# Kernel optimization log

Measured on AMD Instinct MI355X. Metric: run time of the kernel, lower is better.

## Reference

```python
import jax, jax.numpy as jnp
import numpy as np

B, S, HIDDEN = 1, 2048, 3584
NH, NKV, HD = 16, 8, 256
N_REP = NH // NKV
EPS = 1e-6
SCALING = 256.0 ** -0.5  # query_pre_attn_scalar=256
SOFTCAP = 50.0
NEG = -1e9


def rmsnorm(x, w):
    # Gemma RMSNorm with unit offset, computed in fp32
    xf = x.astype(jnp.float32)
    n = xf * jax.lax.rsqrt(jnp.mean(xf * xf, axis=-1, keepdims=True) + EPS)
    return (n * (1.0 + w.astype(jnp.float32))).astype(x.dtype)


def rope(x, cos, sin):
    # x: [B,S,H,D]; gemma pairs (x[:D/2], x[D/2:]) as complex (rotate-half)
    x1, x2 = jnp.split(x, 2, axis=-1)
    c = cos[None, :, None, :]
    s = sin[None, :, None, :]
    return jnp.concatenate([x1 * c - x2 * s, x1 * s + x2 * c], axis=-1).astype(x.dtype)


def setup_inputs() -> dict:
    key = jax.random.key(0)
    ks = jax.random.split(key, 6)
    hidden_states = jax.random.normal(ks[0], (B, S, HIDDEN), jnp.float32)
    w_qkv = jax.random.normal(ks[1], ((NH + 2 * NKV) * HD, HIDDEN), jnp.float32) * 0.02
    w_o = jax.random.normal(ks[2], (HIDDEN, NH * HD), jnp.float32) * 0.02
    q_norm_w = jax.random.normal(ks[3], (HD,), jnp.float32) * 0.1
    k_norm_w = jax.random.normal(ks[4], (HD,), jnp.float32) * 0.1
    k_cache = jnp.zeros((B, S, NKV, HD), jnp.float32)
    v_cache = jnp.zeros((B, S, NKV, HD), jnp.float32)
    kv_write_indices = jnp.arange(S, dtype=jnp.int32)
    # rotary tables, theta=10000
    inv_freq = 1.0 / (10000.0 ** (np.arange(0, HD, 2, dtype=np.float32) / HD))
    t = np.arange(S, dtype=np.float32)
    freqs = np.outer(t, inv_freq)  # [S, HD/2]
    cos = jnp.asarray(np.cos(freqs), jnp.float32)
    sin = jnp.asarray(np.sin(freqs), jnp.float32)
    # causal additive mask [1,1,S,S]
    causal = np.tril(np.ones((S, S), dtype=bool))
    mask = jnp.asarray(np.where(causal, 0.0, NEG).astype(np.float32))[None, None]
    return {"hidden_states": hidden_states, "cos": cos, "sin": sin,
            "kv_write_indices": kv_write_indices, "k_cache": k_cache,
            "v_cache": v_cache, "mask": mask, "w_qkv": w_qkv, "w_o": w_o,
            "q_norm_w": q_norm_w, "k_norm_w": k_norm_w}


def reference(hidden_states, cos, sin, kv_write_indices, k_cache, v_cache,
              mask, w_qkv, w_o, q_norm_w, k_norm_w):
    qkv = jnp.einsum('bsh,oh->bso', hidden_states, w_qkv)
    q_size, kv_size = NH * HD, NKV * HD
    xq = qkv[..., :q_size].reshape(B, S, NH, HD)
    xk = qkv[..., q_size:q_size + kv_size].reshape(B, S, NKV, HD)
    xv = qkv[..., q_size + kv_size:].reshape(B, S, NKV, HD)
    xq = rmsnorm(xq, q_norm_w)
    xk = rmsnorm(xk, k_norm_w)
    xq = rope(xq, cos, sin)
    xk = rope(xk, cos, sin)
    # KV cache write (index_copy_ along dim 1)
    kc = k_cache.at[:, kv_write_indices].set(xk)
    vc = v_cache.at[:, kv_write_indices].set(xv)
    # GQA expand
    key = jnp.repeat(kc, N_REP, axis=2)   # [B,S,NH,HD]
    val = jnp.repeat(vc, N_REP, axis=2)
    q = xq.transpose(0, 2, 1, 3) * SCALING  # [B,NH,S,HD]
    k = key.transpose(0, 2, 1, 3)
    v = val.transpose(0, 2, 1, 3)
    scores = jnp.einsum('bhqd,bhkd->bhqk', q, k)
    scores = jnp.tanh(scores / SOFTCAP) * SOFTCAP  # logit softcapping
    scores = scores + mask
    p = jax.nn.softmax(scores, axis=-1)
    out = jnp.einsum('bhqk,bhkd->bhqd', p, v)
    out = out.transpose(0, 2, 1, 3).reshape(B, S, NH * HD)
    return jnp.einsum('bsd,hd->bsh', out, w_o)
```

## Files before the change

kernel.cpp:

```cpp
#include <hip/hip_runtime.h>

typedef __bf16 bf16;
typedef __bf16 bf16x4 __attribute__((ext_vector_type(4)));
typedef __bf16 bf16x8 __attribute__((ext_vector_type(8)));
typedef float f32x4 __attribute__((ext_vector_type(4)));

#define S_LEN 2048
#define HID   3584
#define NHEADS 16
#define NKVH   8
#define HDIM   256
#define QKV_O  8192
#define O_IN   4096

typedef const __attribute__((address_space(1))) void* gp_t;
typedef __attribute__((address_space(3))) void* sp_t;

__device__ __forceinline__ void async16(const void* g, void* s) {
  __builtin_amdgcn_global_load_lds((gp_t)g, (sp_t)s, 16, 0, 0);
}

__device__ __forceinline__ f32x4 mfma16(bf16x8 a, bf16x8 b, f32x4 c) {
  return __builtin_amdgcn_mfma_f32_16x16x32_bf16(a, b, c, 0, 0, 0);
}

__global__ __launch_bounds__(256) void cast_kernel(const float* __restrict__ in,
                                                   bf16* __restrict__ out, int n4) {
  int i = blockIdx.x * 256 + threadIdx.x;
  if (i >= n4) return;
  f32x4 v = ((const f32x4*)in)[i];
  bf16x4 o = { (bf16)v[0], (bf16)v[1], (bf16)v[2], (bf16)v[3] };
  ((bf16x4*)out)[i] = o;
}

__global__ __launch_bounds__(256) void gemm_nt(const bf16* __restrict__ A, const bf16* __restrict__ B,
                                               float* __restrict__ C, int M, int N, int K) {
  __shared__ bf16 As[128 * 64];
  __shared__ bf16 Bs[128 * 64];
  int tid = threadIdx.x;
  int lane = tid & 63;
  int bm = blockIdx.y, bn = blockIdx.x;
  int w = tid >> 6, wm = w >> 1, wn = w & 1;
  int fr = lane & 15, fq = lane >> 4;
  int sr = tid >> 3;
  int sc = tid & 7;
  int cg = sc ^ (sr & 7);
  const bf16* Ag = A + (size_t)(bm * 128 + sr) * K + cg * 8;
  const bf16* Bg = B + (size_t)(bn * 128 + sr) * K + cg * 8;
  bf16* Asl = &As[sr * 64 + sc * 8];
  bf16* Bsl = &Bs[sr * 64 + sc * 8];
  const bf16* Af = &As[(wm * 64 + fr) * 64];
  const bf16* Bf = &Bs[(wn * 64 + fr) * 64];
  int fsw = fr & 7;
  int fo0 = ((fq ^ fsw) * 8);
  int fo1 = (((4 + fq) ^ fsw) * 8);
  f32x4 acc[4][4];
#pragma unroll
  for (int i = 0; i < 4; i++)
#pragma unroll
    for (int j = 0; j < 4; j++) { f32x4 z = {0.f, 0.f, 0.f, 0.f}; acc[i][j] = z; }
  for (int k0 = 0; k0 < K; k0 += 64) {
    __syncthreads();
#pragma unroll
    for (int p = 0; p < 4; p++) {
      async16(Ag + k0 + (size_t)(p * 32) * K, Asl + p * 32 * 64);
      async16(Bg + k0 + (size_t)(p * 32) * K, Bsl + p * 32 * 64);
    }
    __syncthreads();
#pragma unroll
    for (int ks = 0; ks < 2; ks++) {
      int fo = ks ? fo1 : fo0;
      bf16x8 a[4], b[4];
#pragma unroll
      for (int t = 0; t < 4; t++) a[t] = *(const bf16x8*)(Af + t * 16 * 64 + fo);
#pragma unroll
      for (int t = 0; t < 4; t++) b[t] = *(const bf16x8*)(Bf + t * 16 * 64 + fo);
#pragma unroll
      for (int i = 0; i < 4; i++)
#pragma unroll
        for (int j = 0; j < 4; j++) acc[i][j] = mfma16(a[i], b[j], acc[i][j]);
    }
  }
  int row0 = bm * 128 + wm * 64 + fq * 4;
  int col0 = bn * 128 + wn * 64 + fr;
#pragma unroll
  for (int i = 0; i < 4; i++)
#pragma unroll
    for (int j = 0; j < 4; j++)
#pragma unroll
      for (int r = 0; r < 4; r++)
        C[(size_t)(row0 + i * 16 + r) * N + col0 + j * 16] = acc[i][j][r];
}

__global__ __launch_bounds__(256) void qk_norm_rope(const float* __restrict__ qkv,
                                                    const float* __restrict__ cosb,
                                                    const float* __restrict__ sinb,
                                                    const float* __restrict__ qw,
                                                    const float* __restrict__ kw,
                                                    bf16* __restrict__ qout,
                                                    bf16* __restrict__ kout) {
  int s = blockIdx.x;
  int lane = threadIdx.x & 63;
  int w = threadIdx.x >> 6;
  int d0 = lane * 4;
  int dr = d0 & 127;
  f32x4 cv = *(const f32x4*)(cosb + s * 128 + dr);
  f32x4 sv = *(const f32x4*)(sinb + s * 128 + dr);
  bool hi = lane >= 32;
#pragma unroll
  for (int r = 0; r < 6; r++) {
    int head = r * 4 + w;
    const float* x = qkv + (size_t)s * QKV_O + head * HDIM + d0;
    f32x4 v = *(const f32x4*)x;
    float ss = v[0] * v[0] + v[1] * v[1] + v[2] * v[2] + v[3] * v[3];
#pragma unroll
    for (int off = 32; off > 0; off >>= 1) ss += __shfl_xor(ss, off);
    float scale = rsqrtf(ss * (1.0f / HDIM) + 1e-6f);
    bool isq = head < NHEADS;
    const float* wn = isq ? qw : kw;
    f32x4 wv = *(const f32x4*)(wn + d0);
    float y[4], o[4];
#pragma unroll
    for (int i = 0; i < 4; i++) y[i] = v[i] * scale * (1.0f + wv[i]);
#pragma unroll
    for (int i = 0; i < 4; i++) {
      float py = __shfl_xor(y[i], 32);
      o[i] = hi ? (py * sv[i] + y[i] * cv[i]) : (y[i] * cv[i] - py * sv[i]);
    }
    float mult = isq ? 0.0625f : 1.0f;
    bf16x4 ov = { (bf16)(o[0] * mult), (bf16)(o[1] * mult), (bf16)(o[2] * mult), (bf16)(o[3] * mult) };
    if (isq) *(bf16x4*)(qout + ((size_t)head * S_LEN + s) * HDIM + d0) = ov;
    else     *(bf16x4*)(kout + ((size_t)(head - NHEADS) * S_LEN + s) * HDIM + d0) = ov;
  }
}

__global__ __launch_bounds__(256) void v_transpose(const float* __restrict__ qkv, bf16* __restrict__ vt) {
  __shared__ float tile[64][65];
  int dt = blockIdx.x, st = blockIdx.y, h = blockIdx.z;
  int t = threadIdx.x;
  int d0 = dt * 64, s0 = st * 64;
#pragma unroll
  for (int i = 0; i < 16; i++) {
    int idx = i * 256 + t;
    int r = idx >> 6, c = idx & 63;
    tile[r][c] = qkv[(size_t)(s0 + r) * QKV_O + 6144 + h * HDIM + d0 + c];
  }
  __syncthreads();
#pragma unroll
  for (int i = 0; i < 16; i++) {
    int idx = i * 256 + t;
    int dr = idx >> 6, sc = idx & 63;
    vt[((size_t)h * HDIM + d0 + dr) * S_LEN + s0 + sc] = (bf16)tile[sc][dr];
  }
}

#define PSTRIDE 40
__global__ __launch_bounds__(256) void attn_kernel(const bf16* __restrict__ q,
                                                   const bf16* __restrict__ kx,
                                                   const bf16* __restrict__ vt,
                                                   bf16* __restrict__ aout) {
  __shared__ bf16 kt[32 * 256];
  __shared__ bf16 vtile[256 * 32];
  __shared__ bf16 pbuf[4][16 * PSTRIDE];
  int h = blockIdx.x;
  int y = blockIdx.y;
  int qt = (y < 16) ? y : 47 - y;
  int kvh = h >> 1;
  int tid = threadIdx.x;
  int lane = tid & 63, w = tid >> 6;
  int fr = lane & 15, fq = lane >> 4;
  int qs = qt * 64;
  bf16x8 qf[8];
  const bf16* qb = q + ((size_t)h * S_LEN + qs + w * 16 + fr) * HDIM + fq * 8;
#pragma unroll
  for (int i = 0; i < 8; i++) qf[i] = *(const bf16x8*)(qb + i * 32);
  f32x4 acc[16];
#pragma unroll
  for (int i = 0; i < 16; i++) { f32x4 z = {0.f, 0.f, 0.f, 0.f}; acc[i] = z; }
  float lsum[4] = {0.f, 0.f, 0.f, 0.f};
  int krow = w * 2 + (lane >> 5);
  int kcolr = (lane & 31) * 8;
  const bf16* kg = kx + (size_t)kvh * S_LEN * HDIM;
  int vd = w * 16 + (lane >> 2);
  int vsw = (vd >> 1) & 3;
  int vcl = (lane & 3) * 8;
  int vcg = (((lane & 3) ^ vsw) * 8);
  const bf16* vg = vt + (size_t)kvh * HDIM * S_LEN;
  int rot0 = (fq * 8 - fr * 8) & 255;
  int rot1 = (fq * 8 - fr * 8 - 128) & 255;
  const bf16* kt0 = &kt[fr * 256];
  const bf16* kt1 = &kt[(16 + fr) * 256];
  int fsw = (fr >> 1) & 3;
  int kmax = qs + 64;
  for (int k0 = 0; k0 < kmax; k0 += 32) {
    __syncthreads();
#pragma unroll
    for (int p = 0; p < 4; p++) {
      int r = p * 8 + krow;
      int gc = (kcolr + r * 8) & 255;
      async16(kg + (size_t)(k0 + r) * HDIM + gc, &kt[r * 256 + kcolr]);
      int d = p * 64 + vd;
      async16(vg + (size_t)d * S_LEN + k0 + vcg, &vtile[d * 32 + vcl]);
    }
    __syncthreads();
    f32x4 s0 = {0.f, 0.f, 0.f, 0.f}, s1 = {0.f, 0.f, 0.f, 0.f};
#pragma unroll
    for (int kk = 0; kk < 8; kk++) {
      bf16x8 b0 = *(const bf16x8*)(kt0 + ((kk * 32 + rot0) & 255));
      bf16x8 b1 = *(const bf16x8*)(kt1 + ((kk * 32 + rot1) & 255));
      s0 = mfma16(qf[kk], b0, s0);
      s1 = mfma16(qf[kk], b1, s1);
    }
#pragma unroll
    for (int reg = 0; reg < 4; reg++) {
      int rowg = qs + w * 16 + fq * 4 + reg;
      float u0 = __builtin_amdgcn_exp2f(0.057707802f * s0[reg]);
      float u1 = __builtin_amdgcn_exp2f(0.057707802f * s1[reg]);
      float p0 = __builtin_amdgcn_exp2f(28.853901f - 144.26950f * __builtin_amdgcn_rcpf(u0 + 1.0f));
      float p1 = __builtin_amdgcn_exp2f(28.853901f - 144.26950f * __builtin_amdgcn_rcpf(u1 + 1.0f));
      p0 = (k0 + fr <= rowg) ? p0 : 0.0f;
      p1 = (k0 + 16 + fr <= rowg) ? p1 : 0.0f;
      lsum[reg] += p0 + p1;
      pbuf[w][(fq * 4 + reg) * PSTRIDE + fr] = (bf16)p0;
      pbuf[w][(fq * 4 + reg) * PSTRIDE + 16 + fr] = (bf16)p1;
    }
    bf16x8 pf = *(const bf16x8*)&pbuf[w][fr * PSTRIDE + fq * 8];
#pragma unroll
    for (int ct = 0; ct < 16; ct++) {
      bf16x8 vf = *(const bf16x8*)&vtile[(ct * 16 + fr) * 32 + (fq ^ fsw) * 8];
      acc[ct] = mfma16(pf, vf, acc[ct]);
    }
  }
  float rl[4];
#pragma unroll
  for (int reg = 0; reg < 4; reg++) {
    float l = lsum[reg];
    l += __shfl_xor(l, 1);
    l += __shfl_xor(l, 2);
    l += __shfl_xor(l, 4);
    l += __shfl_xor(l, 8);
    rl[reg] = 1.0f / l;
  }
#pragma unroll
  for (int ct = 0; ct < 16; ct++)
#pragma unroll
    for (int reg = 0; reg < 4; reg++)
      aout[(size_t)(qs + w * 16 + fq * 4 + reg) * O_IN + h * HDIM + ct * 16 + fr] =
          (bf16)(acc[ct][reg] * rl[reg]);
}

extern "C" void kernel_launch(void* const* d_in, const int* in_sizes, int n_in,
                              void* d_out, int out_size, void* d_ws, size_t ws_size,
                              hipStream_t stream) {
  const float* hidden = (const float*)d_in[0];
  const float* cosb   = (const float*)d_in[1];
  const float* sinb   = (const float*)d_in[2];
  const float* wqkv   = (const float*)d_in[7];
  const float* wo     = (const float*)d_in[8];
  const float* qnw    = (const float*)d_in[9];
  const float* knw    = (const float*)d_in[10];
  float* out = (float*)d_out;
  char* ws = (char*)d_ws;
  bf16*  h_bf    = (bf16*)(ws + 0);
  bf16*  wqkv_bf = (bf16*)(ws + 14680064);
  bf16*  wo_bf   = (bf16*)(ws + 73400320);
  float* qkv     = (float*)(ws + 102760448);
  bf16*  qb      = (bf16*)(ws + 169869312);
  bf16*  kb      = (bf16*)(ws + 186646528);
  bf16*  vtb     = (bf16*)(ws + 195035136);
  bf16*  attnb   = (bf16*)(ws + 203423744);

  cast_kernel<<<7168, 256, 0, stream>>>(hidden, h_bf, 1835008);
  cast_kernel<<<28672, 256, 0, stream>>>(wqkv, wqkv_bf, 7340032);
  cast_kernel<<<14336, 256, 0, stream>>>(wo, wo_bf, 3670016);
  gemm_nt<<<dim3(64, 16), 256, 0, stream>>>(h_bf, wqkv_bf, qkv, 2048, 8192, 3584);
  qk_norm_rope<<<2048, 256, 0, stream>>>(qkv, cosb, sinb, qnw, knw, qb, kb);
  v_transpose<<<dim3(4, 32, 8), 256, 0, stream>>>(qkv, vtb);
  attn_kernel<<<dim3(16, 32), 256, 0, stream>>>(qb, kb, vtb, attnb);
  gemm_nt<<<dim3(28, 16), 256, 0, stream>>>(attnb, wo_bf, out, 2048, 3584, 4096);
}
```

Measured before the change: 652.7 us.

## Add 256x256-tile 8-wave pipelined GEMM for the QKV projection

Adds a new NT GEMM kernel with 256x256 output tiles, 512 threads and double-buffered LDS filled by async global-to-LDS loads, interleaving staging with MFMA phases and raising MFMA wave priority. It also remaps block IDs so neighbouring blocks spread across XCD groups. The QKV projection now uses this kernel in place of the 128x128 one, aiming for higher arithmetic intensity and better overlap of loads with compute. The grid shrinks to 256 blocks, so there is less latency hiding between blocks, the tiles use a lot of LDS and registers, and the fixed barrier schedule is fragile.

New measurement: 614.2 us. 5.9% less time.

```diff
diff --git a/kernel.cpp b/kernel.cpp
--- a/kernel.cpp
+++ b/kernel.cpp
@@ -31,6 +31,135 @@
   f32x4 v = ((const f32x4*)in)[i];
   bf16x4 o = { (bf16)v[0], (bf16)v[1], (bf16)v[2], (bf16)v[3] };
   ((bf16x4*)out)[i] = o;
+}
+
+__global__ __launch_bounds__(512, 2) void gemm_nt_8p(const bf16* __restrict__ A,
+                                                     const bf16* __restrict__ B,
+                                                     float* __restrict__ C,
+                                                     int M, int N, int K) {
+  __shared__ bf16 As0[256 * 64];
+  __shared__ bf16 Bs0[256 * 64];
+  __shared__ bf16 As1[256 * 64];
+  __shared__ bf16 Bs1[256 * 64];
+  int tid = threadIdx.x;
+  int lane = tid & 63;
+  int w = tid >> 6;
+  int wm = w >> 2, wn = w & 3;
+  int nbn = N >> 8;
+  int lid = blockIdx.x;
+  int oid = (lid & 7) * ((int)gridDim.x >> 3) + (lid >> 3);
+  int bm = oid / nbn;
+  int bn = oid - bm * nbn;
+  int srow = tid >> 3, schunk = tid & 7;
+  int gcol = (schunk ^ (srow & 7)) * 8;
+  const bf16* Ag = A + (size_t)(bm * 256 + srow) * K + gcol;
+  const bf16* Bg = B + (size_t)(bn * 256 + srow) * K + gcol;
+  int soff = srow * 64 + schunk * 8;
+  int fr = lane & 15, fq = lane >> 4;
+  int c0 = ((fq) ^ (fr & 7)) * 8;
+  int c1 = ((4 + fq) ^ (fr & 7)) * 8;
+  const int arow = (wm * 128 + fr) * 64;
+  const int brow = (wn * 64 + fr) * 64;
+
+  f32x4 acc[8][4];
+#pragma unroll
+  for (int i = 0; i < 8; i++)
+#pragma unroll
+    for (int j = 0; j < 4; j++) { f32x4 z = {0.f, 0.f, 0.f, 0.f}; acc[i][j] = z; }
+  bf16x8 a[8], b[8];
+
+#define STG(gb, lb, kk, half) do {                                    \
+    const bf16* _g = (gb) + (size_t)((half) * 128) * K + (kk);        \
+    bf16* _l = (lb) + (half) * 128 * 64 + soff;                       \
+    async16(_g, _l);                                                  \
+    async16(_g + (size_t)64 * K, _l + 64 * 64);                       \
+  } while (0)
+#define LDA8(base, mg) do {                                           \
+    const bf16* _p = (base) + arow + (mg) * 64 * 64;                  \
+    _Pragma("unroll")                                                 \
+    for (int i = 0; i < 4; i++) {                                     \
+      a[i * 2 + 0] = *(const bf16x8*)(_p + i * 16 * 64 + c0);         \
+      a[i * 2 + 1] = *(const bf16x8*)(_p + i * 16 * 64 + c1);         \
+    }                                                                 \
+  } while (0)
+#define LDB4(base, jh) do {                                           \
+    const bf16* _p = (base) + brow + (jh) * 32 * 64;                  \
+    _Pragma("unroll")                                                 \
+    for (int j = 0; j < 2; j++) {                                     \
+      b[(jh) * 4 + j * 2 + 0] = *(const bf16x8*)(_p + j * 16 * 64 + c0); \
+      b[(jh) * 4 + j * 2 + 1] = *(const bf16x8*)(_p + j * 16 * 64 + c1); \
+    }                                                                 \
+  } while (0)
+#define MM16(mg, jh) do {                                             \
+    __builtin_amdgcn_s_setprio(1);                                    \
+    _Pragma("unroll")                                                 \
+    for (int i = 0; i < 4; i++) {                                     \
+      acc[(mg) * 4 + i][(jh) * 2 + 0] = mfma16(a[i * 2 + 0], b[(jh) * 4 + 0], acc[(mg) * 4 + i][(jh) * 2 + 0]); \
+      acc[(mg) * 4 + i][(jh) * 2 + 0] = mfma16(a[i * 2 + 1], b[(jh) * 4 + 1], acc[(mg) * 4 + i][(jh) * 2 + 0]); \
+      acc[(mg) * 4 + i][(jh) * 2 + 1] = mfma16(a[i * 2 + 0], b[(jh) * 4 + 2], acc[(mg) * 4 + i][(jh) * 2 + 1]); \
+      acc[(mg) * 4 + i][(jh) * 2 + 1] = mfma16(a[i * 2 + 1], b[(jh) * 4 + 3], acc[(mg) * 4 + i][(jh) * 2 + 1]); \
+    }                                                                 \
+    __builtin_amdgcn_s_setprio(0);                                    \
+  } while (0)
+#define BAR() __builtin_amdgcn_s_barrier()
+#define WAITL() do { asm volatile("s_waitcnt lgkmcnt(0)" ::: "memory"); \
+                     __builtin_amdgcn_sched_barrier(0); } while (0)
+#define WAITV4() asm volatile("s_waitcnt vmcnt(4)" ::: "memory")
+
+  const int nT = K >> 6;
+  const int nIter = K >> 7;
+  STG(Ag, As0, 0, 0); STG(Ag, As0, 0, 1);
+  STG(Bg, Bs0, 0, 0); STG(Bg, Bs0, 0, 1);
+  STG(Bg, Bs1, 64, 0); STG(Bg, Bs1, 64, 1);
+  WAITV4();
+  BAR();
+
+  for (int t = 0; t < nIter; t++) {
+    int T = 2 * t;
+    int kA1 = (T + 1) * 64;
+    int t2 = T + 2; if (t2 > nT - 1) t2 = nT - 1;
+    int t3 = T + 3; if (t3 > nT - 1) t3 = nT - 1;
+    int k2 = t2 * 64, k3 = t3 * 64;
+    LDA8(As0, 0); LDB4(Bs0, 0);
+    STG(Ag, As1, kA1, 0);
+    BAR(); WAITL(); MM16(0, 0); BAR();
+    LDB4(Bs0, 1);
+    STG(Ag, As1, kA1, 1);
+    BAR(); WAITL(); MM16(0, 1); BAR();
+    LDA8(As0, 1);
+    STG(Bg, Bs0, k2, 0);
+    BAR(); WAITL(); MM16(1, 0); BAR();
+    STG(Bg, Bs0, k2, 1);
+    BAR(); MM16(1, 1); WAITV4(); BAR();
+    LDA8(As1, 0); LDB4(Bs1, 0);
+    STG(Ag, As0, k2, 0);
+    BAR(); WAITL(); MM16(0, 0); BAR();
+    LDB4(Bs1, 1);
+    STG(Ag, As0, k2, 1);
+    BAR(); WAITL(); MM16(0, 1); BAR();
+    LDA8(As1, 1);
+    STG(Bg, Bs1, k3, 0);
+    BAR(); WAITL(); MM16(1, 0); BAR();
+    STG(Bg, Bs1, k3, 1);
+    BAR(); MM16(1, 1); WAITV4(); BAR();
+  }
+#undef STG
+#undef LDA8
+#undef LDB4
+#undef MM16
+#undef BAR
+#undef WAITL
+#undef WAITV4
+
+  int row0 = bm * 256 + wm * 128 + fq * 4;
+  int col0 = bn * 256 + wn * 64 + fr;
+#pragma unroll
+  for (int i = 0; i < 8; i++)
+#pragma unroll
+    for (int j = 0; j < 4; j++)
+#pragma unroll
+      for (int r = 0; r < 4; r++)
+        C[(size_t)(row0 + i * 16 + r) * N + col0 + j * 16] = acc[i][j][r];
 }
 
 __global__ __launch_bounds__(256) void gemm_nt(const bf16* __restrict__ A, const bf16* __restrict__ B,
@@ -273,7 +402,7 @@
   cast_kernel<<<7168, 256, 0, stream>>>(hidden, h_bf, 1835008);
   cast_kernel<<<28672, 256, 0, stream>>>(wqkv, wqkv_bf, 7340032);
   cast_kernel<<<14336, 256, 0, stream>>>(wo, wo_bf, 3670016);
-  gemm_nt<<<dim3(64, 16), 256, 0, stream>>>(h_bf, wqkv_bf, qkv, 2048, 8192, 3584);
+  gemm_nt_8p<<<256, 512, 0, stream>>>(h_bf, wqkv_bf, qkv, 2048, 8192, 3584);
   qk_norm_rope<<<2048, 256, 0, stream>>>(qkv, cosb, sinb, qnw, knw, qb, kb);
   v_transpose<<<dim3(4, 32, 8), 256, 0, stream>>>(qkv, vtb);
   attn_kernel<<<dim3(16, 32), 256, 0, stream>>>(qb, kb, vtb, attnb);
```

## Replace GEMMs with 256x256 double-buffered 8-wave pipeline and split-K output projection

Applied to the files above, without the earlier changes.

Replaces the simple 128x128 GEMM with a 512-thread kernel that computes 256x256 tiles. It double-buffers LDS, overlaps async global-to-LDS loads with MFMA work using explicit waitcnt, barriers and setprio, and remaps block IDs so nearby blocks share tiles in cache. The output projection is split into two K halves to fill more CUs, with partial results written to workspace and summed by an extra add kernel. This trades extra fp32 partial-buffer traffic and one more launch for higher MFMA utilisation and better occupancy.

New measurement: 580.0 us. 11.1% less time.

```diff
diff --git a/kernel.cpp b/kernel.cpp
--- a/kernel.cpp
+++ b/kernel.cpp
@@ -33,63 +33,172 @@
   ((bf16x4*)out)[i] = o;
 }
 
-__global__ __launch_bounds__(256) void gemm_nt(const bf16* __restrict__ A, const bf16* __restrict__ B,
-                                               float* __restrict__ C, int M, int N, int K) {
-  __shared__ bf16 As[128 * 64];
-  __shared__ bf16 Bs[128 * 64];
+__global__ __launch_bounds__(256) void add2_kernel(const float* __restrict__ a,
+                                                   const float* __restrict__ b,
+                                                   float* __restrict__ o, int n4) {
+  int i = blockIdx.x * 256 + threadIdx.x;
+  if (i >= n4) return;
+  f32x4 x = ((const f32x4*)a)[i];
+  f32x4 y = ((const f32x4*)b)[i];
+  ((f32x4*)o)[i] = x + y;
+}
+
+#define GSTG(gb, lb, kk, half, LDAB) do {                              \
+    const bf16* _g = (gb) + (size_t)((half) * 128) * (LDAB) + (kk);    \
+    bf16* _l = (lb) + (half) * 128 * 64 + soff;                        \
+    async16(_g, _l);                                                   \
+    async16(_g + (size_t)64 * (LDAB), _l + 64 * 64);                   \
+  } while (0)
+#define LD12(ab, bb, cx, ar, br) do {                                  \
+    const bf16* _pa = (ab) + arow;                                     \
+    const bf16* _pb = (bb) + brow;                                     \
+    _Pragma("unroll")                                                  \
+    for (int _i = 0; _i < 8; _i++) ar[_i] = *(const bf16x8*)(_pa + _i * 16 * 64 + (cx)); \
+    _Pragma("unroll")                                                  \
+    for (int _j = 0; _j < 4; _j++) br[_j] = *(const bf16x8*)(_pb + _j * 16 * 64 + (cx)); \
+  } while (0)
+#define MM32(ar, br) do {                                              \
+    __builtin_amdgcn_s_setprio(1);                                     \
+    _Pragma("unroll")                                                  \
+    for (int _i = 0; _i < 8; _i++)                                     \
+      _Pragma("unroll")                                                \
+      for (int _j = 0; _j < 4; _j++)                                   \
+        acc[_i][_j] = mfma16(ar[_i], br[_j], acc[_i][_j]);             \
+    __builtin_amdgcn_s_setprio(0);                                     \
+  } while (0)
+#define BARS() do { __builtin_amdgcn_s_barrier(); __builtin_amdgcn_sched_barrier(0); } while (0)
+#define LGKM0() asm volatile("s_waitcnt lgkmcnt(0)" ::: "memory")
+#define WAITV8() asm volatile("s_waitcnt vmcnt(8)" ::: "memory")
+
+#define GEMM_PIPE_BODY(LDAB)                                           \
+  f32x4 acc[8][4];                                                     \
+  _Pragma("unroll")                                                    \
+  for (int i = 0; i < 8; i++)                                          \
+    _Pragma("unroll")                                                  \
+    for (int j = 0; j < 4; j++) { f32x4 z = {0.f, 0.f, 0.f, 0.f}; acc[i][j] = z; } \
+  bf16x8 a0[8], b0[4], a1[8], b1[4];                                   \
+  const int nT = K >> 6;                                               \
+  const int nIter = K >> 7;                                            \
+  GSTG(Ag, As0, 0, 0, LDAB); GSTG(Ag, As0, 0, 1, LDAB);                \
+  GSTG(Bg, Bs0, 0, 0, LDAB); GSTG(Bg, Bs0, 0, 1, LDAB);                \
+  GSTG(Ag, As1, 64, 0, LDAB); GSTG(Ag, As1, 64, 1, LDAB);              \
+  GSTG(Bg, Bs1, 64, 0, LDAB); GSTG(Bg, Bs1, 64, 1, LDAB);              \
+  WAITV8();                                                            \
+  BARS();                                                              \
+  LD12(As0, Bs0, c0, a0, b0);                                          \
+  for (int t = 0; t < nIter; t++) {                                    \
+    int t2 = 2 * t + 2; if (t2 > nT - 1) t2 = nT - 1;                  \
+    int t3 = 2 * t + 3; if (t3 > nT - 1) t3 = nT - 1;                  \
+    int k2 = t2 * 64, k3 = t3 * 64;                                    \
+              \
+    LD12(As0, Bs0, c1, a1, b1);                                        \
+    MM32(a0, b0);                                                      \
+    LGKM0();                                                           \
+    BARS();                                                            \
+    \
+    GSTG(Ag, As0, k2, 0, LDAB); GSTG(Ag, As0, k2, 1, LDAB);            \
+    GSTG(Bg, Bs0, k2, 0, LDAB); GSTG(Bg, Bs0, k2, 1, LDAB);            \
+    MM32(a1, b1);                                                      \
+    WAITV8();                                                          \
+    BARS();                                                            \
+    LD12(As1, Bs1, c0, a0, b0);                                        \
+                                             \
+    LD12(As1, Bs1, c1, a1, b1);                                        \
+    MM32(a0, b0);                                                      \
+    LGKM0();                                                           \
+    BARS();                                                            \
+                                                              \
+    GSTG(Ag, As1, k3, 0, LDAB); GSTG(Ag, As1, k3, 1, LDAB);            \
+    GSTG(Bg, Bs1, k3, 0, LDAB); GSTG(Bg, Bs1, k3, 1, LDAB);            \
+    MM32(a1, b1);                                                      \
+    WAITV8();                                                          \
+    BARS();                                                            \
+    LD12(As0, Bs0, c0, a0, b0);                                        \
+  }
+
+__global__ __launch_bounds__(512, 2) void gemm_nt_8p(const bf16* __restrict__ A,
+                                                     const bf16* __restrict__ B,
+                                                     float* __restrict__ C,
+                                                     int M, int N, int K) {
+  __shared__ bf16 As0[256 * 64];
+  __shared__ bf16 Bs0[256 * 64];
+  __shared__ bf16 As1[256 * 64];
+  __shared__ bf16 Bs1[256 * 64];
   int tid = threadIdx.x;
   int lane = tid & 63;
-  int bm = blockIdx.y, bn = blockIdx.x;
-  int w = tid >> 6, wm = w >> 1, wn = w & 1;
+  int w = tid >> 6;
+  int wm = w >> 2, wn = w & 3;
+  int lid = blockIdx.x;
+  int oid = (lid & 7) * 32 + (lid >> 3);
+  int rect = oid >> 5, ri = oid & 31;
+  int bm = (rect & 3) * 2 + (ri >> 4);
+  int bn = (rect >> 2) * 16 + (ri & 15);
+  int srow = tid >> 3, schunk = tid & 7;
+  int gcol = (schunk ^ (srow & 7)) * 8;
+  const bf16* Ag = A + (size_t)(bm * 256 + srow) * K + gcol;
+  const bf16* Bg = B + (size_t)(bn * 256 + srow) * K + gcol;
+  int soff = srow * 64 + schunk * 8;
   int fr = lane & 15, fq = lane >> 4;
-  int sr = tid >> 3;
-  int sc = tid & 7;
-  int cg = sc ^ (sr & 7);
-  const bf16* Ag = A + (size_t)(bm * 128 + sr) * K + cg * 8;
-  const bf16* Bg = B + (size_t)(bn * 128 + sr) * K + cg * 8;
-  bf16* Asl = &As[sr * 64 + sc * 8];
-  bf16* Bsl = &Bs[sr * 64 + sc * 8];
-  const bf16* Af = &As[(wm * 64 + fr) * 64];
-  const bf16* Bf = &Bs[(wn * 64 + fr) * 64];
-  int fsw = fr & 7;
-  int fo0 = ((fq ^ fsw) * 8);
-  int fo1 = (((4 + fq) ^ fsw) * 8);
-  f32x4 acc[4][4];
-#pragma unroll
-  for (int i = 0; i < 4; i++)
-#pragma unroll
-    for (int j = 0; j < 4; j++) { f32x4 z = {0.f, 0.f, 0.f, 0.f}; acc[i][j] = z; }
-  for (int k0 = 0; k0 < K; k0 += 64) {
-    __syncthreads();
-#pragma unroll
-    for (int p = 0; p < 4; p++) {
-      async16(Ag + k0 + (size_t)(p * 32) * K, Asl + p * 32 * 64);
-      async16(Bg + k0 + (size_t)(p * 32) * K, Bsl + p * 32 * 64);
-    }
-    __syncthreads();
-#pragma unroll
-    for (int ks = 0; ks < 2; ks++) {
-      int fo = ks ? fo1 : fo0;
-      bf16x8 a[4], b[4];
-#pragma unroll
-      for (int t = 0; t < 4; t++) a[t] = *(const bf16x8*)(Af + t * 16 * 64 + fo);
-#pragma unroll
-      for (int t = 0; t < 4; t++) b[t] = *(const bf16x8*)(Bf + t * 16 * 64 + fo);
-#pragma unroll
-      for (int i = 0; i < 4; i++)
-#pragma unroll
-        for (int j = 0; j < 4; j++) acc[i][j] = mfma16(a[i], b[j], acc[i][j]);
-    }
-  }
-  int row0 = bm * 128 + wm * 64 + fq * 4;
-  int col0 = bn * 128 + wn * 64 + fr;
-#pragma unroll
-  for (int i = 0; i < 4; i++)
+  int c0 = ((fq) ^ (fr & 7)) * 8;
+  int c1 = ((4 + fq) ^ (fr & 7)) * 8;
+  const int arow = (wm * 128 + fr) * 64;
+  const int brow = (wn * 64 + fr) * 64;
+
+  GEMM_PIPE_BODY(K)
+
+  int row0 = bm * 256 + wm * 128 + fq * 4;
+  int col0 = bn * 256 + wn * 64 + fr;
+#pragma unroll
+  for (int i = 0; i < 8; i++)
 #pragma unroll
     for (int j = 0; j < 4; j++)
 #pragma unroll
       for (int r = 0; r < 4; r++)
         C[(size_t)(row0 + i * 16 + r) * N + col0 + j * 16] = acc[i][j][r];
+}
+
+__global__ __launch_bounds__(512, 2) void gemm_nt_8p_ks(const bf16* __restrict__ A,
+                                                        const bf16* __restrict__ B,
+                                                        float* __restrict__ C,
+                                                        int M, int N, int K, int lda) {
+  __shared__ bf16 As0[256 * 64];
+  __shared__ bf16 Bs0[256 * 64];
+  __shared__ bf16 As1[256 * 64];
+  __shared__ bf16 Bs1[256 * 64];
+  int tid = threadIdx.x;
+  int lane = tid & 63;
+  int w = tid >> 6;
+  int wm = w >> 2, wn = w & 3;
+  int lid = blockIdx.x;
+  int ks = lid >= 112;
+  int l2 = lid - ks * 112;
+  int oid = (l2 & 7) * 14 + (l2 >> 3);
+  int bm = oid / 14;
+  int bn = oid - bm * 14;
+  int kbase = ks * K;
+  float* Cp = C + (size_t)ks * M * N;
+  int srow = tid >> 3, schunk = tid & 7;
+  int gcol = (schunk ^ (srow & 7)) * 8;
+  const bf16* Ag = A + (size_t)(bm * 256 + srow) * lda + kbase + gcol;
+  const bf16* Bg = B + (size_t)(bn * 256 + srow) * lda + kbase + gcol;
+  int soff = srow * 64 + schunk * 8;
+  int fr = lane & 15, fq = lane >> 4;
+  int c0 = ((fq) ^ (fr & 7)) * 8;
+  int c1 = ((4 + fq) ^ (fr & 7)) * 8;
+  const int arow = (wm * 128 + fr) * 64;
+  const int brow = (wn * 64 + fr) * 64;
+
+  GEMM_PIPE_BODY(lda)
+
+  int row0 = bm * 256 + wm * 128 + fq * 4;
+  int col0 = bn * 256 + wn * 64 + fr;
+#pragma unroll
+  for (int i = 0; i < 8; i++)
+#pragma unroll
+    for (int j = 0; j < 4; j++)
+#pragma unroll
+      for (int r = 0; r < 4; r++)
+        Cp[(size_t)(row0 + i * 16 + r) * N + col0 + j * 16] = acc[i][j][r];
 }
 
 __global__ __launch_bounds__(256) void qk_norm_rope(const float* __restrict__ qkv,
@@ -269,13 +378,16 @@
   bf16*  kb      = (bf16*)(ws + 186646528);
   bf16*  vtb     = (bf16*)(ws + 195035136);
   bf16*  attnb   = (bf16*)(ws + 203423744);
+  float* part0   = (float*)(ws + 102760448);
+  float* part1   = part0 + (size_t)2048 * 3584;
 
   cast_kernel<<<7168, 256, 0, stream>>>(hidden, h_bf, 1835008);
   cast_kernel<<<28672, 256, 0, stream>>>(wqkv, wqkv_bf, 7340032);
   cast_kernel<<<14336, 256, 0, stream>>>(wo, wo_bf, 3670016);
-  gemm_nt<<<dim3(64, 16), 256, 0, stream>>>(h_bf, wqkv_bf, qkv, 2048, 8192, 3584);
+  gemm_nt_8p<<<256, 512, 0, stream>>>(h_bf, wqkv_bf, qkv, 2048, 8192, 3584);
   qk_norm_rope<<<2048, 256, 0, stream>>>(qkv, cosb, sinb, qnw, knw, qb, kb);
   v_transpose<<<dim3(4, 32, 8), 256, 0, stream>>>(qkv, vtb);
   attn_kernel<<<dim3(16, 32), 256, 0, stream>>>(qb, kb, vtb, attnb);
-  gemm_nt<<<dim3(28, 16), 256, 0, stream>>>(attnb, wo_bf, out, 2048, 3584, 4096);
-}
+  gemm_nt_8p_ks<<<224, 512, 0, stream>>>(attnb, wo_bf, part0, 2048, 3584, 2048, 4096);
+  add2_kernel<<<7168, 256, 0, stream>>>(part0, part1, out, 1835008);
+}
```
